# Optimization experiments

Measured on AMD Instinct MI355X. Metric: run time of the kernel, lower is better.

## Reference

```python
import jax, jax.numpy as jnp
from jax import lax
import numpy as np

SEQ, B, H = 512, 64, 1024


def setup_inputs() -> dict:
    key = jax.random.key(0)
    k1, k2, k3, k4, k5, k6 = jax.random.split(key, 6)
    hidden = jax.random.normal(k1, (SEQ, B, H), dtype=jnp.float32)
    problem_q = jax.random.normal(k2, (B, H), dtype=jnp.float32)
    s = 1.0 / np.sqrt(H)
    WK = jax.random.uniform(k3, (H, H), minval=-s, maxval=s, dtype=jnp.float32)
    bK = jax.random.uniform(k4, (H,), minval=-s, maxval=s, dtype=jnp.float32)
    WV = jax.random.uniform(k5, (H, H), minval=-s, maxval=s, dtype=jnp.float32)
    bV = jax.random.uniform(k6, (H,), minval=-s, maxval=s, dtype=jnp.float32)
    return {"num_xs": 8, "hidden": hidden, "problem_q": problem_q,
            "WK": WK, "bK": bK, "WV": WV, "bV": bV}


def reference(num_xs, hidden, problem_q, WK, bK, WV, bV):
    # hidden: [S, B, H] -> [B, S, H]
    h = jnp.transpose(hidden, (1, 0, 2))
    k = jnp.einsum('bsh,kh->bsk', h, WK) + bK   # K projection, [B, S, H]
    v = jnp.einsum('bsh,vh->bsv', h, WV) + bV   # V projection, [B, S, H]

    def step(x, _):
        # x: [B, H]; scores over seq positions
        scores = jnp.einsum('bh,bsh->bs', x, k)       # [B, S]
        attn = jax.nn.softmax(scores, axis=-1)
        nx = jnp.einsum('bs,bsh->bh', attn, v)        # [B, H]
        return nx, nx

    _, rest = lax.scan(step, problem_q, None, length=num_xs - 1)  # [num_xs-1, B, H]
    xs = jnp.concatenate([problem_q[None], rest], axis=0)          # [num_xs, B, H]
    return jnp.transpose(xs, (1, 0, 2))                            # [B, num_xs, H]
```

## Files before the change

kernel.cpp:

```cpp
#include <hip/hip_runtime.h>

#define SEQ   512
#define BATCH 64
#define HID   1024
#define NX    8
#define SG    64
#define SROWS (SEQ / SG)

__global__ __launch_bounds__(256) void transpose_k(
    const float* __restrict__ in, float* __restrict__ outT)
{
    __shared__ float tile[32][33];
    const int bx = blockIdx.x * 32, by = blockIdx.y * 32;
    const int tx = threadIdx.x & 31, ty = threadIdx.x >> 5;
    #pragma unroll
    for (int r = ty; r < 32; r += 8)
        tile[r][tx] = in[(size_t)(by + r) * HID + bx + tx];
    __syncthreads();
    #pragma unroll
    for (int r = ty; r < 32; r += 8)
        outT[(size_t)(bx + r) * HID + by + tx] = tile[tx][r];
}

__global__ __launch_bounds__(256) void gemv_y_kernel(
    const float* __restrict__ WK, const float* __restrict__ q,
    const float* __restrict__ opfull, const float* __restrict__ bV,
    float* __restrict__ out, int t, float* __restrict__ y)
{
    __shared__ float xs[HID];
    __shared__ float red[8 * 32];
    const int nc = blockIdx.x, b = blockIdx.y;
    const int tid = threadIdx.x;

    {
        const int j4 = tid * 4;
        float4 v;
        if (t == 1) {
            v = *(const float4*)(q + (size_t)b * HID + j4);
        } else {
            float4 o = *(const float4*)(opfull + (size_t)b * HID + j4);
            float4 bb = *(const float4*)(bV + j4);
            v.x = o.x + bb.x; v.y = o.y + bb.y;
            v.z = o.z + bb.z; v.w = o.w + bb.w;
        }
        *(float4*)(xs + j4) = v;
        if (nc == 0)
            *(float4*)(out + ((size_t)(b * NX + t - 1)) * HID + j4) = v;
    }
    __syncthreads();

    const int nl = tid & 31;
    const int jg = tid >> 5;
    const int n  = nc * 32 + nl;
    const float* __restrict__ wp = WK + (size_t)(jg * 128) * HID + n;
    const float* __restrict__ xr = xs + jg * 128;
    float acc = 0.f;
    #pragma unroll 8
    for (int jj = 0; jj < 128; jj++)
        acc += xr[jj] * wp[(size_t)jj * HID];
    red[jg * 32 + nl] = acc;
    __syncthreads();
    if (tid < 32) {
        float s = 0.f;
        #pragma unroll
        for (int g = 0; g < 8; g++) s += red[g * 32 + tid];
        y[(size_t)b * HID + nc * 32 + tid] = s;
    }
}

__global__ __launch_bounds__(256) void fused_attn_kernel(
    const float* __restrict__ hidden, const float* __restrict__ y,
    float* __restrict__ zp, float* __restrict__ ml)
{
    const int sg = blockIdx.x;
    const int b  = blockIdx.y;
    const int tid = threadIdx.x;
    const int w = tid >> 6, lane = tid & 63;

    __shared__ float part[4 * SROWS];

    const int h4 = tid * 4;
    const float4 yv = *(const float4*)(y + (size_t)b * HID + h4);

    float4 hv[SROWS];
    float p[SROWS];
    #pragma unroll
    for (int r = 0; r < SROWS; r++) {
        hv[r] = *(const float4*)(
            hidden + ((size_t)(sg * SROWS + r) * BATCH + b) * HID + h4);
        p[r] = hv[r].x * yv.x + hv[r].y * yv.y + hv[r].z * yv.z + hv[r].w * yv.w;
    }
    #pragma unroll
    for (int r = 0; r < SROWS; r++) {
        float s = p[r];
        #pragma unroll
        for (int off = 32; off; off >>= 1) s += __shfl_xor(s, off);
        if (lane == 0) part[w * SROWS + r] = s;
    }
    __syncthreads();

    float sc[SROWS], m = -1e30f;
    #pragma unroll
    for (int r = 0; r < SROWS; r++) {
        sc[r] = part[0 * SROWS + r] + part[1 * SROWS + r]
              + part[2 * SROWS + r] + part[3 * SROWS + r];
        m = fmaxf(m, sc[r]);
    }
    float we[SROWS], l = 0.f;
    #pragma unroll
    for (int r = 0; r < SROWS; r++) { we[r] = expf(sc[r] - m); l += we[r]; }

    float4 acc = {0.f, 0.f, 0.f, 0.f};
    #pragma unroll
    for (int r = 0; r < SROWS; r++) {
        acc.x += we[r] * hv[r].x; acc.y += we[r] * hv[r].y;
        acc.z += we[r] * hv[r].z; acc.w += we[r] * hv[r].w;
    }
    *(float4*)(zp + ((size_t)(b * SG + sg)) * HID + h4) = acc;
    if (tid == 0) {
        ml[(b * SG + sg) * 2 + 0] = m;
        ml[(b * SG + sg) * 2 + 1] = l;
    }
}

__global__ __launch_bounds__(256) void z_finalize_kernel(
    const float* __restrict__ zp, const float* __restrict__ ml,
    float* __restrict__ z)
{
    __shared__ float mls[2 * SG];
    __shared__ float es[SG];
    __shared__ float red[4 * 64];
    const int hc = blockIdx.x, b = blockIdx.y;
    const int tid = threadIdx.x;

    if (tid < 2 * SG) mls[tid] = ml[b * 2 * SG + tid];
    __syncthreads();
    float M = -1e30f;
    #pragma unroll
    for (int g = 0; g < SG; g++) M = fmaxf(M, mls[2 * g]);
    if (tid < SG) es[tid] = expf(mls[2 * tid] - M);
    __syncthreads();
    float L = 0.f;
    #pragma unroll
    for (int g = 0; g < SG; g++) L += mls[2 * g + 1] * es[g];
    const float invL = 1.0f / L;

    const int hl = tid & 63;
    const int gq = tid >> 6;
    const int h  = hc * 64 + hl;
    const float* __restrict__ zpp = zp + ((size_t)(b * SG + gq * 16)) * HID + h;
    float acc = 0.f;
    #pragma unroll 4
    for (int g = 0; g < 16; g++)
        acc += zpp[(size_t)g * HID] * es[gq * 16 + g];
    red[gq * 64 + hl] = acc;
    __syncthreads();
    if (tid < 64) {
        float s = red[tid] + red[64 + tid] + red[128 + tid] + red[192 + tid];
        z[(size_t)b * HID + hc * 64 + tid] = s * invL;
    }
}

__global__ __launch_bounds__(256) void gemv_out_kernel(
    const float* __restrict__ WVT, const float* __restrict__ z,
    float* __restrict__ opfull)
{
    __shared__ float zs[HID];
    __shared__ float red[8 * 32];
    const int nc = blockIdx.x, b = blockIdx.y;
    const int tid = threadIdx.x;

    *(float4*)(zs + tid * 4) = *(const float4*)(z + (size_t)b * HID + tid * 4);
    __syncthreads();

    const int nl = tid & 31;
    const int hg = tid >> 5;
    const int n  = nc * 32 + nl;
    const float* __restrict__ wp = WVT + (size_t)(hg * 128) * HID + n;
    const float* __restrict__ zr = zs + hg * 128;
    float acc = 0.f;
    #pragma unroll 8
    for (int hh = 0; hh < 128; hh++)
        acc += zr[hh] * wp[(size_t)hh * HID];
    red[hg * 32 + nl] = acc;
    __syncthreads();
    if (tid < 32) {
        float s = 0.f;
        #pragma unroll
        for (int g = 0; g < 8; g++) s += red[g * 32 + tid];
        opfull[(size_t)b * HID + nc * 32 + tid] = s;
    }
}

__global__ __launch_bounds__(256) void final_out_kernel(
    const float* __restrict__ opfull, const float* __restrict__ bias,
    float* __restrict__ out)
{
    const int idx = blockIdx.x * 256 + threadIdx.x;
    const int b = idx >> 10, n = idx & (HID - 1);
    out[((size_t)b * NX + NX - 1) * HID + n] = opfull[idx] + bias[n];
}

extern "C" void kernel_launch(void* const* d_in, const int* in_sizes, int n_in,
                              void* d_out, int out_size, void* d_ws, size_t ws_size,
                              hipStream_t stream)
{
    const float* hidden = (const float*)d_in[1];
    const float* q      = (const float*)d_in[2];
    const float* WK     = (const float*)d_in[3];
    const float* WV     = (const float*)d_in[5];
    const float* bV     = (const float*)d_in[6];
    float* out = (float*)d_out;

    char* ws = (char*)d_ws;
    float* WVT    = (float*)(ws);
    float* y      = (float*)(ws + (4  << 20));
    float* z      = (float*)(ws + (4  << 20) + (256 << 10));
    float* opfull = (float*)(ws + (5  << 20));
    float* ml     = (float*)(ws + (5  << 20) + (256 << 10));
    float* zp     = (float*)(ws + (6  << 20));

    transpose_k<<<dim3(32, 32), 256, 0, stream>>>(WV, WVT);

    for (int t = 1; t < NX; t++) {
        gemv_y_kernel<<<dim3(32, BATCH), 256, 0, stream>>>(
            WK, q, opfull, bV, out, t, y);
        fused_attn_kernel<<<dim3(SG, BATCH), 256, 0, stream>>>(
            hidden, y, zp, ml);
        z_finalize_kernel<<<dim3(16, BATCH), 256, 0, stream>>>(zp, ml, z);
        gemv_out_kernel<<<dim3(32, BATCH), 256, 0, stream>>>(WVT, z, opfull);
    }
    final_out_kernel<<<(BATCH * HID) / 256, 256, 0, stream>>>(opfull, bV, out);
}
```

Baseline: 405.5 us.

## Fuse softmax merge into output GEMV and use online softmax over fewer seq groups

The attention kernel now gives each block 32 sequence rows, processed in batches of 8 with an online softmax. This cuts the seq groups from 64 to 16 and shrinks the partial-result buffer. The z-finalize kernel is removed: each gemv_out block merges the 16 partials itself before its GEMV, which saves one launch per step. The cost is that every one of the 32 column blocks redoes the merge (redundant zp reads), the attention grid is smaller (1024 blocks), and the GEMV grids are transposed so blocks of the same column chunk run adjacently.

```diff
diff --git a/kernel.cpp b/kernel.cpp
--- a/kernel.cpp
+++ b/kernel.cpp
@@ -4,8 +4,9 @@
 #define BATCH 64
 #define HID   1024
 #define NX    8
-#define SG    64
-#define SROWS (SEQ / SG)
+#define SG    16
+#define SB    8
+#define NBAT  4
 
 __global__ __launch_bounds__(256) void transpose_k(
     const float* __restrict__ in, float* __restrict__ outT)
@@ -28,42 +29,41 @@
     float* __restrict__ out, int t, float* __restrict__ y)
 {
     __shared__ float xs[HID];
-    __shared__ float red[8 * 32];
-    const int nc = blockIdx.x, b = blockIdx.y;
+    __shared__ float red[8][32];
+    const int b = blockIdx.x, nc = blockIdx.y;
     const int tid = threadIdx.x;
+    const int h4 = tid * 4;
 
     {
-        const int j4 = tid * 4;
         float4 v;
         if (t == 1) {
-            v = *(const float4*)(q + (size_t)b * HID + j4);
+            v = *(const float4*)(q + (size_t)b * HID + h4);
         } else {
-            float4 o = *(const float4*)(opfull + (size_t)b * HID + j4);
-            float4 bb = *(const float4*)(bV + j4);
+            float4 o  = *(const float4*)(opfull + (size_t)b * HID + h4);
+            float4 bb = *(const float4*)(bV + h4);
             v.x = o.x + bb.x; v.y = o.y + bb.y;
             v.z = o.z + bb.z; v.w = o.w + bb.w;
         }
-        *(float4*)(xs + j4) = v;
+        *(float4*)(xs + h4) = v;
         if (nc == 0)
-            *(float4*)(out + ((size_t)(b * NX + t - 1)) * HID + j4) = v;
-    }
-    __syncthreads();
-
-    const int nl = tid & 31;
-    const int jg = tid >> 5;
-    const int n  = nc * 32 + nl;
+            *(float4*)(out + ((size_t)(b * NX + t - 1)) * HID + h4) = v;
+    }
+    __syncthreads();
+
+    const int nl = tid & 31, jg = tid >> 5;
+    const int n = nc * 32 + nl;
     const float* __restrict__ wp = WK + (size_t)(jg * 128) * HID + n;
     const float* __restrict__ xr = xs + jg * 128;
     float acc = 0.f;
     #pragma unroll 8
     for (int jj = 0; jj < 128; jj++)
         acc += xr[jj] * wp[(size_t)jj * HID];
-    red[jg * 32 + nl] = acc;
+    red[jg][nl] = acc;
     __syncthreads();
     if (tid < 32) {
         float s = 0.f;
         #pragma unroll
-        for (int g = 0; g < 8; g++) s += red[g * 32 + tid];
+        for (int g = 0; g < 8; g++) s += red[g][tid];
         y[(size_t)b * HID + nc * 32 + tid] = s;
     }
 }
@@ -72,49 +72,55 @@
     const float* __restrict__ hidden, const float* __restrict__ y,
     float* __restrict__ zp, float* __restrict__ ml)
 {
-    const int sg = blockIdx.x;
-    const int b  = blockIdx.y;
+    const int sg = blockIdx.x, b = blockIdx.y;
     const int tid = threadIdx.x;
-    const int w = tid >> 6, lane = tid & 63;
-
-    __shared__ float part[4 * SROWS];
-
+    const int lane = tid & 63, w = tid >> 6;
     const int h4 = tid * 4;
+
+    __shared__ float part[4][SB];
+
     const float4 yv = *(const float4*)(y + (size_t)b * HID + h4);
-
-    float4 hv[SROWS];
-    float p[SROWS];
+    float m = -1e30f, l = 0.f;
+    float4 acc = {0.f, 0.f, 0.f, 0.f};
+
     #pragma unroll
-    for (int r = 0; r < SROWS; r++) {
-        hv[r] = *(const float4*)(
-            hidden + ((size_t)(sg * SROWS + r) * BATCH + b) * HID + h4);
-        p[r] = hv[r].x * yv.x + hv[r].y * yv.y + hv[r].z * yv.z + hv[r].w * yv.w;
-    }
-    #pragma unroll
-    for (int r = 0; r < SROWS; r++) {
-        float s = p[r];
-        #pragma unroll
-        for (int off = 32; off; off >>= 1) s += __shfl_xor(s, off);
-        if (lane == 0) part[w * SROWS + r] = s;
-    }
-    __syncthreads();
-
-    float sc[SROWS], m = -1e30f;
-    #pragma unroll
-    for (int r = 0; r < SROWS; r++) {
-        sc[r] = part[0 * SROWS + r] + part[1 * SROWS + r]
-              + part[2 * SROWS + r] + part[3 * SROWS + r];
-        m = fmaxf(m, sc[r]);
-    }
-    float we[SROWS], l = 0.f;
-    #pragma unroll
-    for (int r = 0; r < SROWS; r++) { we[r] = expf(sc[r] - m); l += we[r]; }
-
-    float4 acc = {0.f, 0.f, 0.f, 0.f};
-    #pragma unroll
-    for (int r = 0; r < SROWS; r++) {
-        acc.x += we[r] * hv[r].x; acc.y += we[r] * hv[r].y;
-        acc.z += we[r] * hv[r].z; acc.w += we[r] * hv[r].w;
+    for (int bb = 0; bb < NBAT; bb++) {
+        float4 hv[SB];
+        float p[SB];
+        #pragma unroll
+        for (int r = 0; r < SB; r++) {
+            const int s = sg * 32 + bb * SB + r;
+            hv[r] = *(const float4*)(hidden + ((size_t)s * BATCH + b) * HID + h4);
+            p[r] = hv[r].x * yv.x + hv[r].y * yv.y
+                 + hv[r].z * yv.z + hv[r].w * yv.w;
+        }
+        #pragma unroll
+        for (int r = 0; r < SB; r++) {
+            float s = p[r];
+            #pragma unroll
+            for (int off = 32; off; off >>= 1) s += __shfl_xor(s, off);
+            if (lane == 0) part[w][r] = s;
+        }
+        __syncthreads();
+        float sc[SB], mb = -1e30f;
+        #pragma unroll
+        for (int r = 0; r < SB; r++) {
+            sc[r] = part[0][r] + part[1][r] + part[2][r] + part[3][r];
+            mb = fmaxf(mb, sc[r]);
+        }
+        __syncthreads();
+        const float newm  = fmaxf(m, mb);
+        const float scale = __expf(m - newm);
+        l *= scale;
+        acc.x *= scale; acc.y *= scale; acc.z *= scale; acc.w *= scale;
+        #pragma unroll
+        for (int r = 0; r < SB; r++) {
+            const float we = __expf(sc[r] - newm);
+            l += we;
+            acc.x += we * hv[r].x; acc.y += we * hv[r].y;
+            acc.z += we * hv[r].z; acc.w += we * hv[r].w;
+        }
+        m = newm;
     }
     *(float4*)(zp + ((size_t)(b * SG + sg)) * HID + h4) = acc;
     if (tid == 0) {
@@ -123,71 +129,59 @@
     }
 }
 
-__global__ __launch_bounds__(256) void z_finalize_kernel(
-    const float* __restrict__ zp, const float* __restrict__ ml,
-    float* __restrict__ z)
-{
+__global__ __launch_bounds__(256) void gemv_out_kernel(
+    const float* __restrict__ WVT, const float* __restrict__ zp,
+    const float* __restrict__ ml, float* __restrict__ opfull)
+{
+    __shared__ float xs[HID];
+    __shared__ float red[8][32];
     __shared__ float mls[2 * SG];
-    __shared__ float es[SG];
-    __shared__ float red[4 * 64];
-    const int hc = blockIdx.x, b = blockIdx.y;
+    const int b = blockIdx.x, nc = blockIdx.y;
     const int tid = threadIdx.x;
+    const int h4 = tid * 4;
 
     if (tid < 2 * SG) mls[tid] = ml[b * 2 * SG + tid];
     __syncthreads();
-    float M = -1e30f;
-    #pragma unroll
-    for (int g = 0; g < SG; g++) M = fmaxf(M, mls[2 * g]);
-    if (tid < SG) es[tid] = expf(mls[2 * tid] - M);
-    __syncthreads();
-    float L = 0.f;
-    #pragma unroll
-    for (int g = 0; g < SG; g++) L += mls[2 * g + 1] * es[g];
-    const float invL = 1.0f / L;
-
-    const int hl = tid & 63;
-    const int gq = tid >> 6;
-    const int h  = hc * 64 + hl;
-    const float* __restrict__ zpp = zp + ((size_t)(b * SG + gq * 16)) * HID + h;
-    float acc = 0.f;
-    #pragma unroll 4
-    for (int g = 0; g < 16; g++)
-        acc += zpp[(size_t)g * HID] * es[gq * 16 + g];
-    red[gq * 64 + hl] = acc;
-    __syncthreads();
-    if (tid < 64) {
-        float s = red[tid] + red[64 + tid] + red[128 + tid] + red[192 + tid];
-        z[(size_t)b * HID + hc * 64 + tid] = s * invL;
-    }
-}
-
-__global__ __launch_bounds__(256) void gemv_out_kernel(
-    const float* __restrict__ WVT, const float* __restrict__ z,
-    float* __restrict__ opfull)
-{
-    __shared__ float zs[HID];
-    __shared__ float red[8 * 32];
-    const int nc = blockIdx.x, b = blockIdx.y;
-    const int tid = threadIdx.x;
-
-    *(float4*)(zs + tid * 4) = *(const float4*)(z + (size_t)b * HID + tid * 4);
-    __syncthreads();
-
-    const int nl = tid & 31;
-    const int hg = tid >> 5;
-    const int n  = nc * 32 + nl;
+
+    {
+        float M = -1e30f;
+        #pragma unroll
+        for (int g = 0; g < SG; g++) M = fmaxf(M, mls[2 * g]);
+        float es[SG], L = 0.f;
+        #pragma unroll
+        for (int g = 0; g < SG; g++) {
+            es[g] = __expf(mls[2 * g] - M);
+            L += mls[2 * g + 1] * es[g];
+        }
+        const float invL = 1.0f / L;
+
+        float4 zv = {0.f, 0.f, 0.f, 0.f};
+        #pragma unroll
+        for (int g = 0; g < SG; g++) {
+            const float4 v = *(const float4*)(
+                zp + ((size_t)(b * SG + g)) * HID + h4);
+            zv.x += es[g] * v.x; zv.y += es[g] * v.y;
+            zv.z += es[g] * v.z; zv.w += es[g] * v.w;
+        }
+        zv.x *= invL; zv.y *= invL; zv.z *= invL; zv.w *= invL;
+        *(float4*)(xs + h4) = zv;
+    }
+    __syncthreads();
+
+    const int nl = tid & 31, hg = tid >> 5;
+    const int n = nc * 32 + nl;
     const float* __restrict__ wp = WVT + (size_t)(hg * 128) * HID + n;
-    const float* __restrict__ zr = zs + hg * 128;
+    const float* __restrict__ zr = xs + hg * 128;
     float acc = 0.f;
     #pragma unroll 8
     for (int hh = 0; hh < 128; hh++)
         acc += zr[hh] * wp[(size_t)hh * HID];
-    red[hg * 32 + nl] = acc;
+    red[hg][nl] = acc;
     __syncthreads();
     if (tid < 32) {
         float s = 0.f;
         #pragma unroll
-        for (int g = 0; g < 8; g++) s += red[g * 32 + tid];
+        for (int g = 0; g < 8; g++) s += red[g][tid];
         opfull[(size_t)b * HID + nc * 32 + tid] = s;
     }
 }
@@ -198,7 +192,7 @@
 {
     const int idx = blockIdx.x * 256 + threadIdx.x;
     const int b = idx >> 10, n = idx & (HID - 1);
-    out[((size_t)b * NX + NX - 1) * HID + n] = opfull[idx] + bias[n];
+    out[((size_t)(b * NX + NX - 1)) * HID + n] = opfull[idx] + bias[n];
 }
 
 extern "C" void kernel_launch(void* const* d_in, const int* in_sizes, int n_in,
@@ -214,21 +208,20 @@
 
     char* ws = (char*)d_ws;
     float* WVT    = (float*)(ws);
-    float* y      = (float*)(ws + (4  << 20));
-    float* z      = (float*)(ws + (4  << 20) + (256 << 10));
-    float* opfull = (float*)(ws + (5  << 20));
-    float* ml     = (float*)(ws + (5  << 20) + (256 << 10));
-    float* zp     = (float*)(ws + (6  << 20));
+    float* zp     = (float*)(ws + (4 << 20));
+    float* y      = (float*)(ws + (8 << 20));
+    float* opfull = (float*)(ws + (8 << 20) + (256 << 10));
+    float* ml     = (float*)(ws + (8 << 20) + (512 << 10));
 
     transpose_k<<<dim3(32, 32), 256, 0, stream>>>(WV, WVT);
 
     for (int t = 1; t < NX; t++) {
-        gemv_y_kernel<<<dim3(32, BATCH), 256, 0, stream>>>(
+        gemv_y_kernel<<<dim3(BATCH, 32), 256, 0, stream>>>(
             WK, q, opfull, bV, out, t, y);
         fused_attn_kernel<<<dim3(SG, BATCH), 256, 0, stream>>>(
             hidden, y, zp, ml);
-        z_finalize_kernel<<<dim3(16, BATCH), 256, 0, stream>>>(zp, ml, z);
-        gemv_out_kernel<<<dim3(32, BATCH), 256, 0, stream>>>(WVT, z, opfull);
+        gemv_out_kernel<<<dim3(BATCH, 32), 256, 0, stream>>>(
+            WVT, zp, ml, opfull);
     }
     final_out_kernel<<<(BATCH * HID) / 256, 256, 0, stream>>>(opfull, bV, out);
 }
```

Measured after the change: 456.5 us. 1.13x slower.
